# Optimization experiments

Measured on AMD Instinct MI355X. Metric: run time of the kernel, lower is better.

## Reference

```python
import jax, jax.numpy as jnp
import numpy as np

DIM_IN = 1024
DIM_QK = 1024
DIM_V = 1024


def setup_inputs() -> dict:
    key = jax.random.key(0)
    ks = jax.random.split(key, 8)
    s = DIM_IN ** -0.5
    return {
        "x": jax.random.normal(ks[0], (16, 2048, DIM_IN), dtype=jnp.float32),
        "encoder_output": jax.random.normal(ks[1], (16, 2048, DIM_IN), dtype=jnp.float32),
        "W_q": jax.random.normal(ks[2], (DIM_IN, DIM_QK), dtype=jnp.float32) * s,
        "b_q": jnp.zeros((DIM_QK,), dtype=jnp.float32),
        "W_k": jax.random.normal(ks[3], (DIM_IN, DIM_QK), dtype=jnp.float32) * s,
        "b_k": jnp.zeros((DIM_QK,), dtype=jnp.float32),
        "W_v": jax.random.normal(ks[4], (DIM_IN, DIM_V), dtype=jnp.float32) * s,
        "b_v": jnp.zeros((DIM_V,), dtype=jnp.float32),
    }


def reference(x, encoder_output, W_q, b_q, W_k, b_k, W_v, b_v):
    # Q: [B, Lq, Dqk]; K, V: [B, Lk, Dqk/Dv]
    Q = x @ W_q + b_q
    K = encoder_output @ W_k + b_k
    V = encoder_output @ W_v + b_v
    # attn_scores: [B, Lq, Lk], scaled by 1/sqrt(Dqk)
    scores = jnp.einsum("bqd,bkd->bqk", Q, K) * (K.shape[-1] ** -0.5)
    weights = jax.nn.softmax(scores, axis=-1)
    H = jnp.einsum("bqk,bkv->bqv", weights, V)  # [B, Lq, Dv]
    return H
```

## Files before the change

### kernel.cpp

```cpp
#include <hip/hip_runtime.h>

typedef _Float16 f16;
typedef __attribute__((ext_vector_type(8))) _Float16 f16x8;
typedef __attribute__((ext_vector_type(4))) float f32x4;

#define MFMA16(a, b, c) __builtin_amdgcn_mfma_f32_16x16x32_f16(a, b, c, 0, 0, 0)

__device__ __forceinline__ void gll16(const void* g, void* l) {
    __builtin_amdgcn_global_load_lds(
        (const __attribute__((address_space(1))) unsigned int*)g,
        (__attribute__((address_space(3))) unsigned int*)l, 16, 0, 0);
}

#define BAR() __builtin_amdgcn_s_barrier()
#define LGKM0() do { asm volatile("s_waitcnt lgkmcnt(0)" ::: "memory"); \
                     __builtin_amdgcn_sched_barrier(0); } while (0)
#define VMC(n)  do { asm volatile("s_waitcnt vmcnt(" #n ")" ::: "memory"); \
                     __builtin_amdgcn_sched_barrier(0); } while (0)

__global__ __launch_bounds__(256) void cvt_f16(
    const float* __restrict__ in, f16* __restrict__ out)
{
    const size_t i = ((size_t)blockIdx.x * 256 + threadIdx.x) * 8;
    float4 a = *(const float4*)(in + i);
    float4 b = *(const float4*)(in + i + 4);
    f16x8 o;
    o[0] = (f16)a.x; o[1] = (f16)a.y; o[2] = (f16)a.z; o[3] = (f16)a.w;
    o[4] = (f16)b.x; o[5] = (f16)b.y; o[6] = (f16)b.z; o[7] = (f16)b.w;
    *(f16x8*)(out + i) = o;
}

__global__ __launch_bounds__(256) void prep_weights(
    const float* __restrict__ Wq, const float* __restrict__ Wk,
    const float* __restrict__ Wv, f16* __restrict__ Wt)
{
    __shared__ float tile[32][33];
    const float* W = blockIdx.z == 0 ? Wq : (blockIdx.z == 1 ? Wk : Wv);
    f16* dst = Wt + (size_t)blockIdx.z * 1024 * 1024;
    const int tx = threadIdx.x & 31, ty = threadIdx.x >> 5;
    const int n0 = blockIdx.x * 32, k0 = blockIdx.y * 32;
#pragma unroll
    for (int i = 0; i < 4; i++)
        tile[ty + i * 8][tx] = W[(size_t)(k0 + ty + i * 8) * 1024 + n0 + tx];
    __syncthreads();
#pragma unroll
    for (int i = 0; i < 4; i++)
        dst[(size_t)(n0 + ty + i * 8) * 1024 + k0 + tx] = (f16)tile[tx][ty + i * 8];
}

template <int KD, int EPI>
__global__ __launch_bounds__(512, 2) void gemm8(
    const f16* __restrict__ Ab, const f16* __restrict__ Bb,
    const float* __restrict__ b0, const float* __restrict__ b1, float scale,
    void* __restrict__ C0, void* __restrict__ C1, float* __restrict__ aux,
    size_t strA, size_t strB, size_t strC, int ldc, int nbx, int nby)
{
    __shared__ f16 shA[2][256 * 64];
    __shared__ f16 shB[2][256 * 64];

    int id = blockIdx.x;
    {
        const int chunk = (int)gridDim.x >> 3;
        id = (id & 7) * chunk + (id >> 3);
    }
    const int by = id % nby;
    const int r2 = id / nby;
    const int bx = r2 % nbx;
    const int z  = r2 / nbx;
    const int bm = bx * 256, bn = by * 256;

    const f16* A = Ab + (size_t)z * strA;
    const f16* B = Bb + (size_t)z * strB;

    const int t = threadIdx.x, lane = t & 63, wid = t >> 6;
    const int wr = wid >> 2, wc = wid & 3;
    const int fr = lane & 15, kb = (lane >> 4) * 16;
    const int sw = (fr & 7) << 4;

    const int lsr = lane >> 3;
    const int lsc = ((lane & 7) * 16) ^ (lsr << 4);
    const int a_  = wid * 8;
    const int bq_ = (wid >> 2) * 64 + (wid & 3) * 8;
    const f16* aT = A + (size_t)(bm + lsr) * KD + (lsc >> 1);
    const f16* bT = B + (size_t)(bn + lsr) * KD + (lsc >> 1);

#define STAGE(d, kt)                                                          \
    do {                                                                      \
        const f16* As_ = aT + (size_t)(kt) * 64;                              \
        const f16* Bs_ = bT + (size_t)(kt) * 64;                              \
        f16* da_ = &shA[d][0];                                                \
        f16* db_ = &shB[d][0];                                                \
        gll16(As_ + (size_t)(a_)*KD,        da_ + (a_)*64);                   \
        gll16(As_ + (size_t)(128 + a_)*KD,  da_ + (128 + a_)*64);             \
        gll16(As_ + (size_t)(64 + a_)*KD,   da_ + (64 + a_)*64);              \
        gll16(As_ + (size_t)(192 + a_)*KD,  da_ + (192 + a_)*64);             \
        gll16(Bs_ + (size_t)(bq_)*KD,       db_ + (bq_)*64);                  \
        gll16(Bs_ + (size_t)(128 + bq_)*KD, db_ + (128 + bq_)*64);            \
        gll16(Bs_ + (size_t)(32 + bq_)*KD,  db_ + (32 + bq_)*64);             \
        gll16(Bs_ + (size_t)(160 + bq_)*KD, db_ + (160 + bq_)*64);            \
    } while (0)

    f16x8 af[2][4];
    f16x8 bf[2][2][2];
    f32x4 acc[8][4] = {};

#define LDA(mh)                                                               \
    _Pragma("unroll") for (int kk_ = 0; kk_ < 2; ++kk_)                       \
    _Pragma("unroll") for (int i_ = 0; i_ < 4; ++i_)                          \
        af[kk_][i_] = *(const f16x8*)(sAc +                                   \
            (wr * 128 + (mh) * 64 + i_ * 16 + fr) * 128 +                     \
            (((kk_ << 6) | kb) ^ sw));

#define LDB(nh)                                                               \
    _Pragma("unroll") for (int kk_ = 0; kk_ < 2; ++kk_)                       \
    _Pragma("unroll") for (int j_ = 0; j_ < 2; ++j_)                          \
        bf[nh][kk_][j_] = *(const f16x8*)(sBc +                               \
            (wc * 64 + (nh) * 32 + j_ * 16 + fr) * 128 +                      \
            (((kk_ << 6) | kb) ^ sw));

#define MM(mh, nh)                                                            \
    __builtin_amdgcn_s_setprio(1);                                            \
    _Pragma("unroll") for (int kk_ = 0; kk_ < 2; ++kk_)                       \
    _Pragma("unroll") for (int i_ = 0; i_ < 4; ++i_)                          \
    _Pragma("unroll") for (int j_ = 0; j_ < 2; ++j_)                          \
        acc[(mh) * 4 + i_][(nh) * 2 + j_] =                                   \
            MFMA16(af[kk_][i_], bf[nh][kk_][j_],                              \
                   acc[(mh) * 4 + i_][(nh) * 2 + j_]);                        \
    __builtin_amdgcn_s_setprio(0);

    constexpr int NT = KD / 64;

    STAGE(0, 0);
    VMC(0);
    BAR();

    for (int ti = 0; ti < NT - 1; ++ti) {
        const int c = ti & 1;
        const char* sAc = (const char*)&shA[c][0];
        const char* sBc = (const char*)&shB[c][0];
        STAGE(c ^ 1, ti + 1);
        LDB(0); LDB(1); LDA(0);
        LGKM0();
        MM(0, 0); MM(0, 1);
        LDA(1);
        LGKM0();
        MM(1, 1); MM(1, 0);
        VMC(0);
        BAR();
    }
    {
        const int c = (NT - 1) & 1;
        const char* sAc = (const char*)&shA[c][0];
        const char* sBc = (const char*)&shB[c][0];
        LDB(0); LDB(1); LDA(0);
        LGKM0();
        MM(0, 0); MM(0, 1);
        LDA(1);
        LGKM0();
        MM(1, 1); MM(1, 0);
    }

    const int fc = lane & 15, rq = (lane >> 4) * 4;

    if constexpr (EPI == 2) {
        BAR();
        float* part = (float*)&shA[0][0];
        f16* Sp = (f16*)C0 + (size_t)z * strC;
#pragma unroll
        for (int mi = 0; mi < 8; ++mi)
#pragma unroll
            for (int r = 0; r < 4; ++r) {
                const int rl = wr * 128 + mi * 16 + rq + r;
                float ps = 0.f;
#pragma unroll
                for (int nj = 0; nj < 4; ++nj) {
                    const int col = bn + wc * 64 + nj * 16 + fc;
                    f16 eh = (f16)__expf(acc[mi][nj][r]);
                    ps += (float)eh;
                    Sp[(size_t)(bm + rl) * ldc + col] = eh;
                }
#pragma unroll
                for (int o = 1; o < 16; o <<= 1) ps += __shfl_xor(ps, o);
                if (fc == 0) part[rl * 4 + wc] = ps;
            }
        BAR();
        if (t < 256) {
            const float4 p4 = *(const float4*)(part + t * 4);
            aux[((size_t)z * 2048 + bm + t) * 8 + by] = p4.x + p4.y + p4.z + p4.w;
        }
        return;
    }

#pragma unroll
    for (int nj = 0; nj < 4; ++nj) {
        const int col = bn + wc * 64 + nj * 16 + fc;
        float bv_ = 0.f;
        if constexpr (EPI == 0) bv_ = b0[col];
        if constexpr (EPI == 1) bv_ = (col < 1024) ? b0[col] : b1[col - 1024];
#pragma unroll
        for (int mi = 0; mi < 8; ++mi)
#pragma unroll
            for (int r = 0; r < 4; ++r) {
                const int row = bm + wr * 128 + mi * 16 + rq + r;
                float v = acc[mi][nj][r];
                if constexpr (EPI == 0) v = (v + bv_) * scale;
                if constexpr (EPI == 1) v = v + bv_;
                if constexpr (EPI == 3) v *= aux[(size_t)z * 2048 + row];
                if constexpr (EPI == 0) {
                    ((f16*)C0)[(size_t)row * ldc + col] = (f16)v;
                } else if constexpr (EPI == 1) {
                    if (col < 1024)
                        ((f16*)C0)[(size_t)row * 1024 + col] = (f16)v;
                    else
                        ((f16*)C1)[(size_t)(row >> 11) * 2048 * 1024 +
                                   (size_t)(col - 1024) * 2048 + (row & 2047)] = (f16)v;
                } else {
                    ((float*)C0 + (size_t)z * strC)[(size_t)row * ldc + col] = v;
                }
            }
    }
#undef STAGE
#undef LDA
#undef LDB
#undef MM
}

__global__ __launch_bounds__(256) void rowinv_k(
    const float* __restrict__ part, float* __restrict__ inv)
{
    const int q = blockIdx.x * 256 + threadIdx.x;
    const float4* p = (const float4*)(part + (size_t)q * 8);
    const float4 a = p[0], b = p[1];
    inv[q] = 1.0f / (a.x + a.y + a.z + a.w + b.x + b.y + b.z + b.w);
}

extern "C" void kernel_launch(void* const* d_in, const int* in_sizes, int n_in,
                              void* d_out, int out_size, void* d_ws, size_t ws_size,
                              hipStream_t stream)
{
    const float* x   = (const float*)d_in[0];
    const float* enc = (const float*)d_in[1];
    const float* Wq  = (const float*)d_in[2];
    const float* bq  = (const float*)d_in[3];
    const float* Wk  = (const float*)d_in[4];
    const float* bk  = (const float*)d_in[5];
    const float* Wv  = (const float*)d_in[6];
    const float* bv  = (const float*)d_in[7];

    const size_t TOK = (size_t)16 * 2048;
    f16* Qh = (f16*)d_ws;
    f16* Kh = Qh + TOK * 1024;
    f16* Vt = Kh + TOK * 1024;
    f16* Wt = Vt + TOK * 1024;
    f16* S  = Wt + (size_t)3 * 1024 * 1024;
    f16* Xh = S;
    f16* Eh = S + TOK * 1024;
    float* Ppart = (float*)Wt;
    float* Rinv  = Ppart + TOK * 8;

    cvt_f16<<<16384, 256, 0, stream>>>(x,   Xh);
    cvt_f16<<<16384, 256, 0, stream>>>(enc, Eh);

    prep_weights<<<dim3(32, 32, 3), 256, 0, stream>>>(Wq, Wk, Wv, Wt);

    gemm8<1024, 0><<<512, 512, 0, stream>>>(
        Xh, Wt, bq, nullptr, 0.03125f, Qh, nullptr, nullptr,
        0, 0, 0, 1024, 128, 4);

    gemm8<1024, 1><<<1024, 512, 0, stream>>>(
        Eh, Wt + (size_t)1024 * 1024, bk, bv, 1.0f, Kh, Vt, nullptr,
        0, 0, 0, 1024, 128, 8);

    gemm8<1024, 2><<<1024, 512, 0, stream>>>(
        Qh, Kh, nullptr, nullptr, 1.0f, S, nullptr, Ppart,
        (size_t)2048 * 1024, (size_t)2048 * 1024, (size_t)2048 * 2048, 2048, 8, 8);

    rowinv_k<<<128, 256, 0, stream>>>(Ppart, Rinv);

    gemm8<2048, 3><<<512, 512, 0, stream>>>(
        S, Vt, nullptr, nullptr, 1.0f, d_out, nullptr, Rinv,
        (size_t)2048 * 2048, (size_t)1024 * 2048, (size_t)2048 * 1024, 1024, 8, 4);
}
```

Before: 777.9 us.

## Restructure GEMM main loop with partial waitcnts and vectorize transposed V stores

Rewrites the double-buffered GEMM loop so the next tile's global-to-LDS prefetch is issued first and only waited on partially (vmcnt(8)), with one barrier before the LDS reads instead of a full drain at the end of each iteration. All A and B fragments are loaded up front into a larger register array, and lgkmcnt(8) lets the first MFMA half start before the second half's LDS reads finish. In the K/V projection epilogue, the transposed V writes become 4-wide f16 vector stores instead of scalar strided stores. The extra fragment registers may raise register pressure and lower occupancy.

Result: faster. 707.5 us (-9.1%).

```diff
diff --git a/kernel.cpp b/kernel.cpp
--- a/kernel.cpp
+++ b/kernel.cpp
@@ -1,6 +1,7 @@
 #include <hip/hip_runtime.h>
 
 typedef _Float16 f16;
+typedef __attribute__((ext_vector_type(4))) _Float16 f16x4;
 typedef __attribute__((ext_vector_type(8))) _Float16 f16x8;
 typedef __attribute__((ext_vector_type(4))) float f32x4;
 
@@ -13,7 +14,7 @@
 }
 
 #define BAR() __builtin_amdgcn_s_barrier()
-#define LGKM0() do { asm volatile("s_waitcnt lgkmcnt(0)" ::: "memory"); \
+#define LGKM(n) do { asm volatile("s_waitcnt lgkmcnt(" #n ")" ::: "memory"); \
                      __builtin_amdgcn_sched_barrier(0); } while (0)
 #define VMC(n)  do { asm volatile("s_waitcnt vmcnt(" #n ")" ::: "memory"); \
                      __builtin_amdgcn_sched_barrier(0); } while (0)
@@ -100,14 +101,14 @@
         gll16(Bs_ + (size_t)(160 + bq_)*KD, db_ + (160 + bq_)*64);            \
     } while (0)
 
-    f16x8 af[2][4];
+    f16x8 af[2][2][4];
     f16x8 bf[2][2][2];
     f32x4 acc[8][4] = {};
 
 #define LDA(mh)                                                               \
     _Pragma("unroll") for (int kk_ = 0; kk_ < 2; ++kk_)                       \
     _Pragma("unroll") for (int i_ = 0; i_ < 4; ++i_)                          \
-        af[kk_][i_] = *(const f16x8*)(sAc +                                   \
+        af[mh][kk_][i_] = *(const f16x8*)(sAc +                               \
             (wr * 128 + (mh) * 64 + i_ * 16 + fr) * 128 +                     \
             (((kk_ << 6) | kb) ^ sw));
 
@@ -124,40 +125,31 @@
     _Pragma("unroll") for (int i_ = 0; i_ < 4; ++i_)                          \
     _Pragma("unroll") for (int j_ = 0; j_ < 2; ++j_)                          \
         acc[(mh) * 4 + i_][(nh) * 2 + j_] =                                   \
-            MFMA16(af[kk_][i_], bf[nh][kk_][j_],                              \
+            MFMA16(af[mh][kk_][i_], bf[nh][kk_][j_],                          \
                    acc[(mh) * 4 + i_][(nh) * 2 + j_]);                        \
     __builtin_amdgcn_s_setprio(0);
 
     constexpr int NT = KD / 64;
 
     STAGE(0, 0);
-    VMC(0);
-    BAR();
-
-    for (int ti = 0; ti < NT - 1; ++ti) {
+
+    for (int ti = 0; ti < NT; ++ti) {
         const int c = ti & 1;
         const char* sAc = (const char*)&shA[c][0];
         const char* sBc = (const char*)&shB[c][0];
-        STAGE(c ^ 1, ti + 1);
-        LDB(0); LDB(1); LDA(0);
-        LGKM0();
+        if (ti + 1 < NT) {
+            STAGE(c ^ 1, ti + 1);
+            VMC(8);
+        } else {
+            VMC(0);
+        }
+        BAR();
+        LDA(0); LDB(0); LDB(1); LDA(1);
+        LGKM(8);
         MM(0, 0); MM(0, 1);
-        LDA(1);
-        LGKM0();
+        LGKM(0);
         MM(1, 1); MM(1, 0);
-        VMC(0);
-        BAR();
-    }
-    {
-        const int c = (NT - 1) & 1;
-        const char* sAc = (const char*)&shA[c][0];
-        const char* sBc = (const char*)&shB[c][0];
-        LDB(0); LDB(1); LDA(0);
-        LGKM0();
-        MM(0, 0); MM(0, 1);
-        LDA(1);
-        LGKM0();
-        MM(1, 1); MM(1, 0);
+        BAR();
     }
 
     const int fc = lane & 15, rq = (lane >> 4) * 4;
@@ -198,7 +190,19 @@
         if constexpr (EPI == 0) bv_ = b0[col];
         if constexpr (EPI == 1) bv_ = (col < 1024) ? b0[col] : b1[col - 1024];
 #pragma unroll
-        for (int mi = 0; mi < 8; ++mi)
+        for (int mi = 0; mi < 8; ++mi) {
+            if constexpr (EPI == 1) {
+                if (col >= 1024) {
+                    const int rowb = bm + wr * 128 + mi * 16 + rq;
+                    f16x4 q;
+#pragma unroll
+                    for (int r = 0; r < 4; ++r) q[r] = (f16)(acc[mi][nj][r] + bv_);
+                    f16* Cp = (f16*)C1 + (size_t)(rowb >> 11) * 2048 * 1024 +
+                              (size_t)(col - 1024) * 2048;
+                    *(f16x4*)&Cp[rowb & 2047] = q;
+                    continue;
+                }
+            }
 #pragma unroll
             for (int r = 0; r < 4; ++r) {
                 const int row = bm + wr * 128 + mi * 16 + rq + r;
@@ -209,15 +213,12 @@
                 if constexpr (EPI == 0) {
                     ((f16*)C0)[(size_t)row * ldc + col] = (f16)v;
                 } else if constexpr (EPI == 1) {
-                    if (col < 1024)
-                        ((f16*)C0)[(size_t)row * 1024 + col] = (f16)v;
-                    else
-                        ((f16*)C1)[(size_t)(row >> 11) * 2048 * 1024 +
-                                   (size_t)(col - 1024) * 2048 + (row & 2047)] = (f16)v;
+                    ((f16*)C0)[(size_t)row * 1024 + col] = (f16)v;
                 } else {
                     ((float*)C0 + (size_t)z * strC)[(size_t)row * ldc + col] = v;
                 }
             }
+        }
     }
 #undef STAGE
 #undef LDA
```
